# Performance work log

Measured on AMD Instinct MI355X. Metric: run time of the kernel, lower is better.

## Reference

```python
import jax, jax.numpy as jnp
import numpy as np


def setup_inputs() -> dict:
    key = jax.random.key(0)
    ks = jax.random.split(key, 4)
    B, T, D, U = 64, 512, 1024, 1024
    scale = 1.0 / np.sqrt(D)
    return {
        "x": jax.random.normal(ks[0], (B, T, D), dtype=jnp.float32),
        "kernel_z": jax.random.normal(ks[1], (D, U), dtype=jnp.float32) * scale,
        "kernel_r": jax.random.normal(ks[2], (D, U), dtype=jnp.float32) * scale,
        "kernel_h": jax.random.normal(ks[3], (D, U), dtype=jnp.float32) * scale,
        "memory_z": jnp.ones((U,), dtype=jnp.float32),
        "memory_r": jnp.ones((U,), dtype=jnp.float32),
        "bias_z": jnp.zeros((U,), dtype=jnp.float32),
        "bias_r": jnp.zeros((U,), dtype=jnp.float32),
        "bias_h": jnp.zeros((U,), dtype=jnp.float32),
    }


def _bru_scan(x, kernel_z, kernel_r, kernel_h, memory_z, memory_r,
              bias_z, bias_r, bias_h):
    B, T, D = x.shape
    U = kernel_z.shape[1]
    # Precompute the three input projections for all timesteps at once
    # (same math as per-step K.dot; hoisted out of the recurrence).
    xz = jnp.einsum('btd,du->btu', x, kernel_z) + bias_z  # [B,T,U]
    xr = jnp.einsum('btd,du->btu', x, kernel_r) + bias_r
    xh = jnp.einsum('btd,du->btu', x, kernel_h) + bias_h

    def step(h, xs):
        xz_t, xr_t, xh_t = xs
        r = jnp.tanh(xr_t + h * memory_r) + 1.0
        z = jax.nn.sigmoid(xz_t + h * memory_z)
        hh = jnp.tanh(xh_t + r * h)
        out = (1.0 - z) * hh + z * h
        return out, out

    h0 = jnp.zeros((B, U), dtype=x.dtype)
    # scan over time axis
    xs = (jnp.swapaxes(xz, 0, 1), jnp.swapaxes(xr, 0, 1), jnp.swapaxes(xh, 0, 1))
    _, outs = jax.lax.scan(step, h0, xs)  # outs: [T,B,U]
    return jnp.swapaxes(outs, 0, 1)  # [B,T,U]


def reference(x, kernel_z, kernel_r, kernel_h, memory_z, memory_r,
              bias_z, bias_r, bias_h):
    return _bru_scan(x, kernel_z, kernel_r, kernel_h, memory_z, memory_r,
                     bias_z, bias_r, bias_h)
```

## Files before the change

kernel.cpp:

```cpp
#include <hip/hip_runtime.h>
#include <cmath>

using f16x8  = __attribute__((ext_vector_type(8))) _Float16;
using f32x16 = __attribute__((ext_vector_type(16))) float;

__device__ __forceinline__ void gld16(void* lds, const void* g) {
    __builtin_amdgcn_global_load_lds(
        (const __attribute__((address_space(1))) unsigned int*)g,
        (__attribute__((address_space(3))) unsigned int*)lds, 16, 0, 0);
}


__global__ __launch_bounds__(256)
void bru_conv_a(const float* __restrict__ x, char* __restrict__ Ablob,
                int T, int D, int Tc, int t0, int Mc)
{
    const int gid = blockIdx.x * 256 + threadIdx.x;
    const int kt = gid / Mc;
    const int m  = gid - kt * Mc;
    const int mt = m >> 8, row = m & 255;

    const long xrow = (long)(m / Tc) * T + t0 + (m % Tc);
    const float* src = x + xrow * (long)D + kt * 32;

    float v[32];
    #pragma unroll
    for (int i = 0; i < 8; ++i)
        *(float4*)&v[i * 4] = *(const float4*)(src + i * 4);

    _Float16 hi[32], lo[32];
    #pragma unroll
    for (int k = 0; k < 32; ++k) {
        hi[k] = (_Float16)v[k];
        lo[k] = (_Float16)(v[k] - (float)hi[k]);
    }

    char* base = Ablob + ((size_t)(mt * 33 + kt)) * 32768 + (size_t)row * 128;
    #pragma unroll
    for (int qe = 0; qe < 8; ++qe) {
        _Float16 o[8];
        #pragma unroll
        for (int j = 0; j < 8; ++j) {
            const int k = qe * 4 + (j >> 1);
            o[j] = (j & 1) ? lo[k] : hi[k];
        }
        *(f16x8*)(base + ((qe ^ (row & 7)) << 4)) = *(f16x8*)o;
    }
}

__global__ __launch_bounds__(256)
void bru_conv_w(const float* __restrict__ wz, const float* __restrict__ wr,
                const float* __restrict__ wh, char* __restrict__ Wblob,
                int D, int U)
{
    const int gid  = blockIdx.x * 256 + threadIdx.x;
    const int blob = gid >> 11;
    const int idx  = gid & 2047;
    const int qe   = idx >> 8;
    const int row  = idx & 255;

    const int nt12 = blob >> 5;
    const int kt   = blob & 31;
    const int g    = nt12 >> 2;
    const int ntl  = nt12 & 3;

    const float* W = (g == 0) ? wz : (g == 1) ? wr : wh;
    const int ucol = ntl * 256 + row;

    _Float16 wf[4];
    #pragma unroll
    for (int jj = 0; jj < 4; ++jj)
        wf[jj] = (_Float16)W[(long)(kt * 32 + qe * 4 + jj) * U + ucol];

    _Float16 o[8];
    #pragma unroll
    for (int j = 0; j < 8; ++j) o[j] = wf[j >> 1];

    *(f16x8*)(Wblob + ((size_t)(nt12 * 33 + kt)) * 32768 + (size_t)row * 128
              + ((qe ^ (row & 7)) << 4)) = *(f16x8*)o;
}

__global__ __launch_bounds__(512, 2)
void bru_gemm_mfma(const char* __restrict__ Ablob, const char* __restrict__ Wblob,
                   const float* __restrict__ bz, const float* __restrict__ br,
                   const float* __restrict__ bh,
                   _Float16* __restrict__ proj,
                   int nmt, int U, int Mc)
{
    __shared__ char sm[131072];

    const int ngrid = gridDim.x;
    const int bid   = blockIdx.x;
    int lid = bid;
    if ((ngrid & 7) == 0) lid = (bid & 7) * (ngrid >> 3) + (bid >> 3);
    const int mt   = lid / 12;
    const int nt12 = lid - mt * 12;
    const int g    = nt12 >> 2;
    const int ntl  = nt12 & 3;

    const int tid  = threadIdx.x;
    const int lane = tid & 63;
    const int w    = tid >> 6;
    const int wm   = w >> 2, wn = w & 3;
    const int l31  = lane & 31;
    const int lhi  = lane >> 5;
    const int r7   = l31 & 7;

    const char* asrc = Ablob + (size_t)(mt * 33) * 32768;
    const char* bsrc = Wblob + (size_t)(nt12 * 33) * 32768;

    const int abase = (wm * 128 + l31) * 128;
    const int bbase = 32768 + (wn * 64 + l31) * 128;

    f32x16 acc[4][2];
    #pragma unroll
    for (int i = 0; i < 4; ++i)
        #pragma unroll
        for (int j = 0; j < 2; ++j) acc[i][j] = (f32x16)0.f;

    #pragma unroll
    for (int c = 0; c < 4; ++c) {
        gld16(sm + c * 8192 + tid * 16,         asrc + c * 8192 + tid * 16);
        gld16(sm + 32768 + c * 8192 + tid * 16, bsrc + c * 8192 + tid * 16);
    }
    __syncthreads();

    for (int kt = 0; kt < 32; ++kt) {
        const int cur = (kt & 1) << 16;
        char* nxt = sm + (cur ^ 65536);
        const char* an = asrc + (size_t)(kt + 1) * 32768;
        const char* bn = bsrc + (size_t)(kt + 1) * 32768;

        #pragma unroll
        for (int c = 0; c < 4; ++c) {
            gld16(nxt + c * 8192 + tid * 16,         an + c * 8192 + tid * 16);
            gld16(nxt + 32768 + c * 8192 + tid * 16, bn + c * 8192 + tid * 16);
        }

        const char* smc = sm + cur;
        #pragma unroll
        for (int ks = 0; ks < 4; ++ks) {
            const int slot = ((ks * 2 + lhi) ^ r7) << 4;
            f16x8 af[4], bf[2];
            #pragma unroll
            for (int i = 0; i < 4; ++i)
                af[i] = *(const f16x8*)(smc + abase + i * 4096 + slot);
            #pragma unroll
            for (int j = 0; j < 2; ++j)
                bf[j] = *(const f16x8*)(smc + bbase + j * 4096 + slot);
            #pragma unroll
            for (int i = 0; i < 4; ++i)
                #pragma unroll
                for (int j = 0; j < 2; ++j)
                    acc[i][j] = __builtin_amdgcn_mfma_f32_32x32x16_f16(
                        af[i], bf[j], acc[i][j], 0, 0, 0);
        }

        __syncthreads();
    }

    const float* bias = (g == 0) ? bz : (g == 1) ? br : bh;
    const int n0 = ntl * 256 + wn * 64;
    float bcol[2];
    #pragma unroll
    for (int j = 0; j < 2; ++j) bcol[j] = bias[n0 + j * 32 + l31];

    _Float16* cbase = proj + (size_t)g * Mc * U + (size_t)n0 + l31;
    #pragma unroll
    for (int i = 0; i < 4; ++i) {
        #pragma unroll
        for (int j = 0; j < 2; ++j) {
            #pragma unroll
            for (int reg = 0; reg < 16; ++reg) {
                const int row = mt * 256 + wm * 128 + i * 32
                              + (reg & 3) + 8 * (reg >> 2) + 4 * lhi;
                cbase[(size_t)row * U + j * 32] = (_Float16)(acc[i][j][reg] + bcol[j]);
            }
        }
    }
}

#define PF 8
__global__ __launch_bounds__(256)
void bru_scan(const _Float16* __restrict__ proj,
              const float* __restrict__ mz, const float* __restrict__ mr,
              float* __restrict__ out,
              float* __restrict__ hstate,
              int B, int T, int U, int Tc, int t0, int Mc)
{
    const int idx = blockIdx.x * blockDim.x + threadIdx.x;
    const int b = idx / U;
    const int u = idx - b * U;

    float h = (t0 == 0) ? 0.f : hstate[idx];
    const float vmz = mz[u];
    const float vmr = mr[u];

    const _Float16* pz = proj + (long)b * Tc * U + u;
    const _Float16* pr = pz + (long)Mc * U;
    const _Float16* ph = pr + (long)Mc * U;
    float* po = out + ((long)b * T + t0) * U + u;

    _Float16 fz[PF], fr[PF], fh[PF];
    #pragma unroll
    for (int i = 0; i < PF; ++i) {
        const long o = (long)((i < Tc) ? i : (Tc - 1)) * U;
        fz[i] = pz[o]; fr[i] = pr[o]; fh[i] = ph[o];
    }

    for (int t = 0; t < Tc; t += PF) {
        #pragma unroll
        for (int i = 0; i < PF; ++i) {
            const float xz = (float)fz[i];
            const float xr = (float)fr[i];
            const float xh = (float)fh[i];
            {
                int tn = t + i + PF; if (tn > Tc - 1) tn = Tc - 1;
                const long o = (long)tn * U;
                fz[i] = pz[o]; fr[i] = pr[o]; fh[i] = ph[o];
            }
            const float e2r = __expf(2.f * (xr + h * vmr));
            const float rr  = 2.f - 2.f / (e2r + 1.f);
            const float zz  = 1.f / (1.f + __expf(-(xz + h * vmz)));
            const float e2h = __expf(2.f * (xh + rr * h));
            const float hh  = 1.f - 2.f / (e2h + 1.f);
            h = (1.f - zz) * hh + zz * h;
            if (t + i < Tc) po[(long)(t + i) * U] = h;
        }
    }
    hstate[idx] = h;
}

extern "C" void kernel_launch(void* const* d_in, const int* in_sizes, int n_in,
                              void* d_out, int out_size, void* d_ws, size_t ws_size,
                              hipStream_t stream)
{
    const float* x  = (const float*)d_in[0];
    const float* wz = (const float*)d_in[1];
    const float* wr = (const float*)d_in[2];
    const float* wh = (const float*)d_in[3];
    const float* mz = (const float*)d_in[4];
    const float* mr = (const float*)d_in[5];
    const float* bz = (const float*)d_in[6];
    const float* br = (const float*)d_in[7];
    const float* bh = (const float*)d_in[8];

    const int B = 64, T = 512, D = 1024, U = 1024;

    const size_t h_bytes = (size_t)B * U * sizeof(float);
    const size_t w_bytes = (size_t)12 * 33 * 32768;

    int Tc = T;
    while (Tc > 4) {
        const int nmt_ = B * Tc / 256;
        const size_t a_bytes_ = (size_t)nmt_ * 33 * 32768;
        const size_t p_bytes_ = 3ull * B * Tc * U * sizeof(_Float16);
        if (h_bytes + w_bytes + a_bytes_ + p_bytes_ <= ws_size) break;
        Tc >>= 1;
    }
    const int nmt = B * Tc / 256;
    const int Mc  = B * Tc;
    const size_t a_bytes = (size_t)nmt * 33 * 32768;

    float*    h_state = (float*)d_ws;
    char*     Wblob   = (char*)d_ws + h_bytes;
    char*     Ablob   = (char*)d_ws + h_bytes + w_bytes;
    _Float16* proj    = (_Float16*)((char*)d_ws + h_bytes + w_bytes + a_bytes);

    bru_conv_w<<<12 * 32 * 2048 / 256, 256, 0, stream>>>(wz, wr, wh, Wblob, D, U);

    for (int t0 = 0; t0 < T; t0 += Tc) {
        bru_conv_a<<<(Mc * 32) / 256, 256, 0, stream>>>(x, Ablob, T, D, Tc, t0, Mc);

        bru_gemm_mfma<<<3 * nmt * 4, 512, 0, stream>>>(
            Ablob, Wblob, bz, br, bh, proj, nmt, U, Mc);

        bru_scan<<<(B * U) / 256, 256, 0, stream>>>(
            proj, mz, mr, (float*)d_out, h_state, B, T, U, Tc, t0, Mc);
    }
}
```

Before: 630.0 us.

## Shrink GEMM tiles to 128x128 with 16x16x32 MFMA and single-buffered LDS

Rewrites the projection GEMM from 256x256 tiles with 512 threads, 32x32 MFMA and double-buffered 128KB LDS to 128x128 tiles with 256 threads, 16x16x32 MFMA and a single 32KB LDS buffer. The A and W blob layouts and the converter kernels change to match, and set_prio is placed around the MFMA bursts. Smaller LDS use and more blocks are meant to raise occupancy and let waves hide latency. In exchange the explicit load/compute overlap from double buffering is dropped, and smaller tiles give less data reuse and more global traffic.

Result: no change. 631.7 us (+0.3%).

```diff
diff --git a/kernel.cpp b/kernel.cpp
--- a/kernel.cpp
+++ b/kernel.cpp
@@ -1,8 +1,8 @@
 #include <hip/hip_runtime.h>
 #include <cmath>
 
-using f16x8  = __attribute__((ext_vector_type(8))) _Float16;
-using f32x16 = __attribute__((ext_vector_type(16))) float;
+using f16x8 = __attribute__((ext_vector_type(8))) _Float16;
+using f32x4 = __attribute__((ext_vector_type(4))) float;
 
 __device__ __forceinline__ void gld16(void* lds, const void* g) {
     __builtin_amdgcn_global_load_lds(
@@ -18,7 +18,7 @@
     const int gid = blockIdx.x * 256 + threadIdx.x;
     const int kt = gid / Mc;
     const int m  = gid - kt * Mc;
-    const int mt = m >> 8, row = m & 255;
+    const int mt = m >> 7, row = m & 127;
 
     const long xrow = (long)(m / Tc) * T + t0 + (m % Tc);
     const float* src = x + xrow * (long)D + kt * 32;
@@ -35,7 +35,7 @@
         lo[k] = (_Float16)(v[k] - (float)hi[k]);
     }
 
-    char* base = Ablob + ((size_t)(mt * 33 + kt)) * 32768 + (size_t)row * 128;
+    char* base = Ablob + ((size_t)(mt * 32 + kt)) * 16384 + (size_t)row * 128;
     #pragma unroll
     for (int qe = 0; qe < 8; ++qe) {
         _Float16 o[8];
@@ -54,18 +54,19 @@
                 int D, int U)
 {
     const int gid  = blockIdx.x * 256 + threadIdx.x;
-    const int blob = gid >> 11;
-    const int idx  = gid & 2047;
-    const int qe   = idx >> 8;
-    const int row  = idx & 255;
-
-    const int nt12 = blob >> 5;
-    const int kt   = blob & 31;
-    const int g    = nt12 >> 2;
-    const int ntl  = nt12 & 3;
+    const int blob = gid >> 10;
+    const int idx  = gid & 1023;
+    const int row  = idx >> 3;
+    const int s    = idx & 7;
+
+    const int g    = blob >> 8;
+    const int rest = blob & 255;
+    const int nt   = rest >> 5;
+    const int kt   = rest & 31;
 
     const float* W = (g == 0) ? wz : (g == 1) ? wr : wh;
-    const int ucol = ntl * 256 + row;
+    const int qe   = s ^ (row & 7);
+    const int ucol = nt * 128 + row;
 
     _Float16 wf[4];
     #pragma unroll
@@ -76,106 +77,98 @@
     #pragma unroll
     for (int j = 0; j < 8; ++j) o[j] = wf[j >> 1];
 
-    *(f16x8*)(Wblob + ((size_t)(nt12 * 33 + kt)) * 32768 + (size_t)row * 128
-              + ((qe ^ (row & 7)) << 4)) = *(f16x8*)o;
-}
-
-__global__ __launch_bounds__(512, 2)
+    *(f16x8*)(Wblob + (size_t)blob * 16384 + (size_t)row * 128 + s * 16)
+        = *(f16x8*)o;
+}
+
+__global__ __launch_bounds__(256)
 void bru_gemm_mfma(const char* __restrict__ Ablob, const char* __restrict__ Wblob,
                    const float* __restrict__ bz, const float* __restrict__ br,
                    const float* __restrict__ bh,
                    _Float16* __restrict__ proj,
                    int nmt, int U, int Mc)
 {
-    __shared__ char sm[131072];
+    __shared__ char sm[32768];
 
     const int ngrid = gridDim.x;
     const int bid   = blockIdx.x;
     int lid = bid;
     if ((ngrid & 7) == 0) lid = (bid & 7) * (ngrid >> 3) + (bid >> 3);
-    const int mt   = lid / 12;
-    const int nt12 = lid - mt * 12;
-    const int g    = nt12 >> 2;
-    const int ntl  = nt12 & 3;
-
-    const int tid  = threadIdx.x;
-    const int lane = tid & 63;
-    const int w    = tid >> 6;
-    const int wm   = w >> 2, wn = w & 3;
-    const int l31  = lane & 31;
-    const int lhi  = lane >> 5;
-    const int r7   = l31 & 7;
-
-    const char* asrc = Ablob + (size_t)(mt * 33) * 32768;
-    const char* bsrc = Wblob + (size_t)(nt12 * 33) * 32768;
-
-    const int abase = (wm * 128 + l31) * 128;
-    const int bbase = 32768 + (wn * 64 + l31) * 128;
-
-    f32x16 acc[4][2];
+    const int per_gate = nmt * 8;
+    const int g  = lid / per_gate;
+    const int r  = lid - g * per_gate;
+    const int mt = r >> 3;
+    const int nt = r & 7;
+
+    const int tid    = threadIdx.x;
+    const int lane   = tid & 63;
+    const int w      = tid >> 6;
+    const int wm     = w >> 1, wn = w & 1;
+    const int lane15 = lane & 15;
+    const int lgrp   = lane >> 4;
+    const int r7     = lane15 & 7;
+
+    const char* asrc = Ablob + (size_t)(mt * 32) * 16384;
+    const char* bsrc = Wblob + (size_t)((g * 8 + nt) * 32) * 16384;
+
+    const int abase = (wm * 64 + lane15) * 128;
+    const int bbase = 16384 + (wn * 64 + lane15) * 128;
+
+    f32x4 acc[4][4];
     #pragma unroll
     for (int i = 0; i < 4; ++i)
         #pragma unroll
-        for (int j = 0; j < 2; ++j) acc[i][j] = (f32x16)0.f;
-
-    #pragma unroll
-    for (int c = 0; c < 4; ++c) {
-        gld16(sm + c * 8192 + tid * 16,         asrc + c * 8192 + tid * 16);
-        gld16(sm + 32768 + c * 8192 + tid * 16, bsrc + c * 8192 + tid * 16);
-    }
-    __syncthreads();
+        for (int j = 0; j < 4; ++j) acc[i][j] = (f32x4)0.f;
 
     for (int kt = 0; kt < 32; ++kt) {
-        const int cur = (kt & 1) << 16;
-        char* nxt = sm + (cur ^ 65536);
-        const char* an = asrc + (size_t)(kt + 1) * 32768;
-        const char* bn = bsrc + (size_t)(kt + 1) * 32768;
-
-        #pragma unroll
-        for (int c = 0; c < 4; ++c) {
-            gld16(nxt + c * 8192 + tid * 16,         an + c * 8192 + tid * 16);
-            gld16(nxt + 32768 + c * 8192 + tid * 16, bn + c * 8192 + tid * 16);
-        }
-
-        const char* smc = sm + cur;
-        #pragma unroll
-        for (int ks = 0; ks < 4; ++ks) {
-            const int slot = ((ks * 2 + lhi) ^ r7) << 4;
-            f16x8 af[4], bf[2];
-            #pragma unroll
-            for (int i = 0; i < 4; ++i)
-                af[i] = *(const f16x8*)(smc + abase + i * 4096 + slot);
-            #pragma unroll
-            for (int j = 0; j < 2; ++j)
-                bf[j] = *(const f16x8*)(smc + bbase + j * 4096 + slot);
-            #pragma unroll
-            for (int i = 0; i < 4; ++i)
+        const char* at = asrc + (size_t)kt * 16384;
+        const char* bt = bsrc + (size_t)kt * 16384;
+
+        #pragma unroll
+        for (int c = 0; c < 4; ++c)
+            gld16(sm + c * 4096 + tid * 16, at + c * 4096 + tid * 16);
+        #pragma unroll
+        for (int c = 0; c < 4; ++c)
+            gld16(sm + 16384 + c * 4096 + tid * 16, bt + c * 4096 + tid * 16);
+        __syncthreads();
+
+        #pragma unroll
+        for (int ks = 0; ks < 2; ++ks) {
+            const int slot = ((ks * 4 + lgrp) ^ r7) << 4;
+            f16x8 af[4], bf[4];
+            #pragma unroll
+            for (int f = 0; f < 4; ++f)
+                af[f] = *(const f16x8*)(sm + abase + f * 2048 + slot);
+            #pragma unroll
+            for (int j = 0; j < 4; ++j)
+                bf[j] = *(const f16x8*)(sm + bbase + j * 2048 + slot);
+            __builtin_amdgcn_s_setprio(1);
+            #pragma unroll
+            for (int f = 0; f < 4; ++f)
                 #pragma unroll
-                for (int j = 0; j < 2; ++j)
-                    acc[i][j] = __builtin_amdgcn_mfma_f32_32x32x16_f16(
-                        af[i], bf[j], acc[i][j], 0, 0, 0);
-        }
-
+                for (int j = 0; j < 4; ++j)
+                    acc[f][j] = __builtin_amdgcn_mfma_f32_16x16x32_f16(
+                        af[f], bf[j], acc[f][j], 0, 0, 0);
+            __builtin_amdgcn_s_setprio(0);
+        }
         __syncthreads();
     }
 
     const float* bias = (g == 0) ? bz : (g == 1) ? br : bh;
-    const int n0 = ntl * 256 + wn * 64;
-    float bcol[2];
-    #pragma unroll
-    for (int j = 0; j < 2; ++j) bcol[j] = bias[n0 + j * 32 + l31];
-
-    _Float16* cbase = proj + (size_t)g * Mc * U + (size_t)n0 + l31;
-    #pragma unroll
-    for (int i = 0; i < 4; ++i) {
-        #pragma unroll
-        for (int j = 0; j < 2; ++j) {
-            #pragma unroll
-            for (int reg = 0; reg < 16; ++reg) {
-                const int row = mt * 256 + wm * 128 + i * 32
-                              + (reg & 3) + 8 * (reg >> 2) + 4 * lhi;
-                cbase[(size_t)row * U + j * 32] = (_Float16)(acc[i][j][reg] + bcol[j]);
-            }
+    const int n0 = nt * 128 + wn * 64;
+    float bcol[4];
+    #pragma unroll
+    for (int j = 0; j < 4; ++j) bcol[j] = bias[n0 + j * 16 + lane15];
+
+    _Float16* cbase = proj + (size_t)g * Mc * U + (size_t)n0 + lane15;
+    #pragma unroll
+    for (int f = 0; f < 4; ++f) {
+        #pragma unroll
+        for (int reg = 0; reg < 4; ++reg) {
+            const int row = mt * 128 + wm * 64 + f * 16 + lgrp * 4 + reg;
+            #pragma unroll
+            for (int j = 0; j < 4; ++j)
+                cbase[(size_t)row * U + j * 16] = (_Float16)(acc[f][j][reg] + bcol[j]);
         }
     }
 }
@@ -248,31 +241,31 @@
     const int B = 64, T = 512, D = 1024, U = 1024;
 
     const size_t h_bytes = (size_t)B * U * sizeof(float);
-    const size_t w_bytes = (size_t)12 * 33 * 32768;
+    const size_t w_bytes = (size_t)768 * 16384;
 
     int Tc = T;
     while (Tc > 4) {
-        const int nmt_ = B * Tc / 256;
-        const size_t a_bytes_ = (size_t)nmt_ * 33 * 32768;
-        const size_t p_bytes_ = 3ull * B * Tc * U * sizeof(_Float16);
+        const int Mc_ = B * Tc;
+        const size_t a_bytes_ = (size_t)Mc_ * 4096;
+        const size_t p_bytes_ = 3ull * Mc_ * U * sizeof(_Float16);
         if (h_bytes + w_bytes + a_bytes_ + p_bytes_ <= ws_size) break;
         Tc >>= 1;
     }
-    const int nmt = B * Tc / 256;
+    const int nmt = B * Tc / 128;
     const int Mc  = B * Tc;
-    const size_t a_bytes = (size_t)nmt * 33 * 32768;
+    const size_t a_bytes = (size_t)Mc * 4096;
 
     float*    h_state = (float*)d_ws;
     char*     Wblob   = (char*)d_ws + h_bytes;
     char*     Ablob   = (char*)d_ws + h_bytes + w_bytes;
     _Float16* proj    = (_Float16*)((char*)d_ws + h_bytes + w_bytes + a_bytes);
 
-    bru_conv_w<<<12 * 32 * 2048 / 256, 256, 0, stream>>>(wz, wr, wh, Wblob, D, U);
+    bru_conv_w<<<768 * 1024 / 256, 256, 0, stream>>>(wz, wr, wh, Wblob, D, U);
 
     for (int t0 = 0; t0 < T; t0 += Tc) {
         bru_conv_a<<<(Mc * 32) / 256, 256, 0, stream>>>(x, Ablob, T, D, Tc, t0, Mc);
 
-        bru_gemm_mfma<<<3 * nmt * 4, 512, 0, stream>>>(
+        bru_gemm_mfma<<<3 * nmt * 8, 256, 0, stream>>>(
             Ablob, Wblob, bz, br, bh, proj, nmt, U, Mc);
 
         bru_scan<<<(B * U) / 256, 256, 0, stream>>>(
```
